# Performance work log

Hardware: AMD Instinct MI355X
Metric: run time of the kernel (lower is better)

Reference implementation:

```python
import jax, jax.numpy as jnp
import numpy as np

B, T, RNN_DIM, EMB_DIM, ATT_DIM = 64, 2048, 1024, 512, 128
N_FILT, KSIZE = 32, 31
PAD = (KSIZE - 1) // 2


def setup_inputs() -> dict:
    key = jax.random.key(0)
    ks = jax.random.split(key, 9)
    return {
        "attention_hidden_state": jax.random.normal(ks[0], (B, RNN_DIM), jnp.float32),
        "memory": jax.random.normal(ks[1], (B, T, EMB_DIM), jnp.float32),
        "processed_memory": jax.random.normal(ks[2], (B, T, ATT_DIM), jnp.float32),
        "attention_weights_cat": jax.random.uniform(ks[3], (B, 2, T), jnp.float32),
        "mask": jnp.zeros((B, T), dtype=bool),
        # learned params (torch Linear stores weight as (out, in))
        "Wq": jax.random.normal(ks[4], (ATT_DIM, RNN_DIM), jnp.float32) * 0.02,
        "conv_w": jax.random.normal(ks[5], (N_FILT, 2, KSIZE), jnp.float32) * 0.1,
        "Wd": jax.random.normal(ks[6], (ATT_DIM, N_FILT), jnp.float32) * 0.1,
        "v": jax.random.normal(ks[7], (1, ATT_DIM), jnp.float32) * 0.1,
    }


def reference(attention_hidden_state, memory, processed_memory,
              attention_weights_cat, mask, Wq, conv_w, Wd, v):
    # processed_query: (B, 1, ATT_DIM)
    pq = jnp.einsum('br,ar->ba', attention_hidden_state, Wq)[:, None, :]
    # location conv: (B, 2, T) -> (B, N_FILT, T), padding keeps length
    loc = jax.lax.conv_general_dilated(
        attention_weights_cat, conv_w,
        window_strides=(1,), padding=[(PAD, PAD)],
        dimension_numbers=('NCH', 'OIH', 'NCH'))
    # transpose to (B, T, N_FILT), dense to (B, T, ATT_DIM)
    loc = jnp.einsum('bft,af->bta', loc, Wd)
    # energies: tanh(pq + loc + pm) @ v^T -> (B, T)
    energies = jnp.einsum('bta,a->bt', jnp.tanh(pq + loc + processed_memory), v[0])
    energies = jnp.where(mask, -jnp.inf, energies)
    attention_weights = jax.nn.softmax(energies, axis=1)
    # context: (B, 1, T) x (B, T, EMB) -> (B, EMB)
    attention_context = jnp.einsum('bt,bte->be', attention_weights, memory)
    return attention_context, attention_weights
```

## Files before the change

### kernel.cpp

```cpp
#include <hip/hip_runtime.h>
#include <hip/hip_bf16.h>
#include <cstdint>

#define BB 64
#define TN 2048
#define RNN 1024
#define EMB 512
#define ATT 128
#define NF 32
#define KS 31
#define PADK 15
#define CKN 62
#define TT 256

__device__ __forceinline__ float fast_rcp(float x) {
#if __has_builtin(__builtin_amdgcn_rcpf)
    return __builtin_amdgcn_rcpf(x);
#else
    return 1.0f / x;
#endif
}

__device__ __forceinline__ float fast_tanh(float x) {
    float s = __expf(2.0f * x);
    return 1.0f - 2.0f * fast_rcp(s + 1.0f);
}

__global__ __launch_bounds__(256) void prep_kernel(
    const float* __restrict__ ahs, const float* __restrict__ Wq,
    const float* __restrict__ conv_w, const float* __restrict__ Wd,
    float* __restrict__ ws_pq, float* __restrict__ ws_U)
{
    int tid = threadIdx.x;
    if (blockIdx.x < BB) {
        int b = blockIdx.x;
        __shared__ float sh[RNN];
        for (int i = tid; i < RNN; i += 256) sh[i] = ahs[b * RNN + i];
        __syncthreads();
        int a = tid & 127, half = tid >> 7;
        const float4* wq4 = (const float4*)(Wq + a * RNN + half * (RNN / 2));
        const float4* sh4 = (const float4*)(sh + half * (RNN / 2));
        float acc = 0.0f;
#pragma unroll 8
        for (int i = 0; i < RNN / 8; ++i) {
            float4 w4 = wq4[i]; float4 h4 = sh4[i];
            acc = fmaf(w4.x, h4.x, acc);
            acc = fmaf(w4.y, h4.y, acc);
            acc = fmaf(w4.z, h4.z, acc);
            acc = fmaf(w4.w, h4.w, acc);
        }
        __shared__ float part[256];
        part[tid] = acc;
        __syncthreads();
        if (half == 0) ws_pq[b * ATT + a] = part[a] + part[a + 128];
    } else {
        __shared__ float sWd[ATT * NF];
        __shared__ float sCw[NF * CKN];
        for (int i = tid; i < ATT * NF; i += 256) sWd[i] = Wd[i];
        for (int i = tid; i < NF * CKN; i += 256) sCw[i] = conv_w[i];
        __syncthreads();
        for (int idx = tid; idx < ATT * CKN; idx += 256) {
            int a = idx / CKN, ck = idx % CKN;
            float acc = 0.0f;
#pragma unroll
            for (int f = 0; f < NF; ++f) acc = fmaf(sWd[a * NF + f], sCw[f * CKN + ck], acc);
            ws_U[idx] = acc;
        }
    }
}

__global__ __launch_bounds__(256) void energies_kernel(
    const float* __restrict__ awc, const float* __restrict__ pm,
    const float* __restrict__ vvec,
    const float* __restrict__ ws_pq, const float* __restrict__ ws_U,
    float* __restrict__ ws_e)
{
    __shared__ float sU[ATT * 63];
    __shared__ float sA[2][TT + 32];
    __shared__ float sPq[ATT];
    int tid = threadIdx.x;
    int b = blockIdx.x, t0 = blockIdx.y * TT;

    for (int idx = tid; idx < ATT * CKN; idx += 256) {
        int a = idx / CKN, ck = idx % CKN;
        sU[a * 63 + ck] = ws_U[idx];
    }
    for (int idx = tid; idx < 2 * (TT + 30); idx += 256) {
        int c = idx / (TT + 30), tt = idx % (TT + 30);
        int t = t0 + tt - PADK;
        sA[c][tt] = (t >= 0 && t < TN) ? awc[(b * 2 + c) * TN + t] : 0.0f;
    }
    if (tid < ATT) sPq[tid] = ws_pq[b * ATT + tid];
    __syncthreads();

    int lane = tid & 63, wv = tid >> 6;
    float v0 = vvec[lane], v1 = vvec[lane + 64];
    float q0 = sPq[lane], q1 = sPq[lane + 64];
    const float* U0 = &sU[lane * 63];
    const float* U1 = &sU[(lane + 64) * 63];
    const float* pmb = pm + (size_t)b * TN * ATT;

    for (int i = 0; i < TT / 4; ++i) {
        int tl = i * 4 + wv;
        int t = t0 + tl;
        float lo0 = 0.0f, lo1 = 0.0f;
#pragma unroll
        for (int c = 0; c < 2; ++c) {
#pragma unroll
            for (int k = 0; k < KS; ++k) {
                float x = sA[c][tl + k];
                lo0 = fmaf(U0[c * KS + k], x, lo0);
                lo1 = fmaf(U1[c * KS + k], x, lo1);
            }
        }
        float p0 = pmb[(size_t)t * ATT + lane];
        float p1 = pmb[(size_t)t * ATT + 64 + lane];
        float e = v0 * fast_tanh(q0 + lo0 + p0) + v1 * fast_tanh(q1 + lo1 + p1);
#pragma unroll
        for (int off = 32; off >= 1; off >>= 1) e += __shfl_xor(e, off, 64);
        if (lane == 0) ws_e[b * TN + t] = e;
    }
}

__global__ __launch_bounds__(256) void softmax_kernel(
    const float* __restrict__ ws_e, const uint8_t* __restrict__ mask,
    float* __restrict__ out_w)
{
    int b = blockIdx.x, tid = threadIdx.x;
    float vals[TN / 256];
    float m = -INFINITY;
#pragma unroll
    for (int i = 0; i < TN / 256; ++i) {
        int t = tid + i * 256;
        float e = ws_e[b * TN + t];
        if (mask[b * TN + t]) e = -INFINITY;
        vals[i] = e;
        m = fmaxf(m, e);
    }
    __shared__ float redm[4];
#pragma unroll
    for (int off = 32; off >= 1; off >>= 1) m = fmaxf(m, __shfl_xor(m, off, 64));
    if ((tid & 63) == 0) redm[tid >> 6] = m;
    __syncthreads();
    m = fmaxf(fmaxf(redm[0], redm[1]), fmaxf(redm[2], redm[3]));

    float s = 0.0f;
#pragma unroll
    for (int i = 0; i < TN / 256; ++i) s += __expf(vals[i] - m);
    __shared__ float reds[4];
#pragma unroll
    for (int off = 32; off >= 1; off >>= 1) s += __shfl_xor(s, off, 64);
    if ((tid & 63) == 0) reds[tid >> 6] = s;
    __syncthreads();
    s = reds[0] + reds[1] + reds[2] + reds[3];
    float inv = 1.0f / s;
#pragma unroll
    for (int i = 0; i < TN / 256; ++i) {
        int t = tid + i * 256;
        out_w[b * TN + t] = __expf(vals[i] - m) * inv;
    }
}

__global__ __launch_bounds__(256) void context_partial_kernel(
    const float* __restrict__ mem, const float* __restrict__ w,
    float* __restrict__ partial, int chunkT)
{
    int b = blockIdx.x, ch = blockIdx.y;
    int tid = threadIdx.x;
    int tc0 = ch * chunkT;
    extern __shared__ float sw[];
    for (int i = tid; i < chunkT; i += 256) sw[i] = w[b * TN + tc0 + i];
    __syncthreads();

    int e4 = tid & 127, sub = tid >> 7;
    const float4* m4 = (const float4*)(mem + ((size_t)(b * TN + tc0)) * EMB);
    float4 acc = make_float4(0.f, 0.f, 0.f, 0.f);
    for (int i = sub; i < chunkT; i += 2) {
        float wt = sw[i];
        float4 mv = m4[(size_t)i * 128 + e4];
        acc.x = fmaf(wt, mv.x, acc.x);
        acc.y = fmaf(wt, mv.y, acc.y);
        acc.z = fmaf(wt, mv.z, acc.z);
        acc.w = fmaf(wt, mv.w, acc.w);
    }
    __shared__ float4 sacc[128];
    if (sub == 1) sacc[e4] = acc;
    __syncthreads();
    if (sub == 0) {
        float4 o = sacc[e4];
        acc.x += o.x; acc.y += o.y; acc.z += o.z; acc.w += o.w;
        ((float4*)partial)[((size_t)ch * BB + b) * 128 + e4] = acc;
    }
}

__global__ __launch_bounds__(256) void context_reduce_kernel(
    const float* __restrict__ partial, float* __restrict__ out_ctx, int nchunk)
{
    int o = blockIdx.x * 256 + threadIdx.x;
    int b = o >> 9, e = o & 511;
    float acc = 0.0f;
    for (int c = 0; c < nchunk; ++c)
        acc += partial[((size_t)c * BB + b) * EMB + e];
    out_ctx[o] = acc;
}

extern "C" void kernel_launch(void* const* d_in, const int* in_sizes, int n_in,
                              void* d_out, int out_size, void* d_ws, size_t ws_size,
                              hipStream_t stream) {
    const float*   ahs  = (const float*)d_in[0];
    const float*   mem  = (const float*)d_in[1];
    const float*   pm   = (const float*)d_in[2];
    const float*   awc  = (const float*)d_in[3];
    const uint8_t* mask = (const uint8_t*)d_in[4];
    const float*   Wq   = (const float*)d_in[5];
    const float*   cw   = (const float*)d_in[6];
    const float*   Wd   = (const float*)d_in[7];
    const float*   v    = (const float*)d_in[8];

    float* out_ctx = (float*)d_out;
    float* out_w   = (float*)d_out + BB * EMB;

    float* ws      = (float*)d_ws;
    float* ws_pq   = ws;
    float* ws_U    = ws + 8192;
    float* ws_e    = ws + 16384;
    float* ws_part = ws + 147456;

    int nchunk = 16;
    while (nchunk > 1 &&
           (size_t)(147456 + (size_t)nchunk * BB * EMB) * 4 > ws_size)
        nchunk >>= 1;
    int chunkT = TN / nchunk;

    prep_kernel<<<BB + 1, 256, 0, stream>>>(ahs, Wq, cw, Wd, ws_pq, ws_U);
    energies_kernel<<<dim3(BB, TN / TT), 256, 0, stream>>>(awc, pm, v, ws_pq, ws_U, ws_e);
    softmax_kernel<<<BB, 256, 0, stream>>>(ws_e, mask, out_w);
    context_partial_kernel<<<dim3(BB, nchunk), 256, chunkT * 4, stream>>>(mem, out_w, ws_part, chunkT);
    context_reduce_kernel<<<(BB * EMB) / 256, 256, 0, stream>>>(ws_part, out_ctx, nchunk);
}
```

Baseline: 496.5 us.

## Register-cache conv weights in energies kernel and fuse softmax into context pass

The energies kernel now keeps each thread's 62 location-conv weights in registers from a transposed global layout, instead of staging the full U matrix in shared memory. Each wave handles one attention half and computes four timesteps per sliding window read from shared memory. Per-half energies are combined through shared memory. Softmax is merged into the context partial kernel: each block recomputes the row max and sum, then writes its own weight chunk, which removes one launch and the reload of the weights. The costs are redundant softmax reductions in every chunk block and higher register pressure, and the workspace-size fallback for the chunk count is dropped.

```diff
diff --git a/kernel.cpp b/kernel.cpp
--- a/kernel.cpp
+++ b/kernel.cpp
@@ -11,7 +11,9 @@
 #define KS 31
 #define PADK 15
 #define CKN 62
-#define TT 256
+#define ETT 256
+#define NCHUNK 16
+#define CHT 128
 
 __device__ __forceinline__ float fast_rcp(float x) {
 #if __has_builtin(__builtin_amdgcn_rcpf)
@@ -29,7 +31,7 @@
 __global__ __launch_bounds__(256) void prep_kernel(
     const float* __restrict__ ahs, const float* __restrict__ Wq,
     const float* __restrict__ conv_w, const float* __restrict__ Wd,
-    float* __restrict__ ws_pq, float* __restrict__ ws_U)
+    float* __restrict__ ws_pq, float* __restrict__ ws_UT)
 {
     int tid = threadIdx.x;
     if (blockIdx.x < BB) {
@@ -60,11 +62,11 @@
         for (int i = tid; i < NF * CKN; i += 256) sCw[i] = conv_w[i];
         __syncthreads();
         for (int idx = tid; idx < ATT * CKN; idx += 256) {
-            int a = idx / CKN, ck = idx % CKN;
+            int a = idx & 127, ck = idx >> 7;
             float acc = 0.0f;
 #pragma unroll
             for (int f = 0; f < NF; ++f) acc = fmaf(sWd[a * NF + f], sCw[f * CKN + ck], acc);
-            ws_U[idx] = acc;
+            ws_UT[idx] = acc;
         }
     }
 }
@@ -72,61 +74,69 @@
 __global__ __launch_bounds__(256) void energies_kernel(
     const float* __restrict__ awc, const float* __restrict__ pm,
     const float* __restrict__ vvec,
-    const float* __restrict__ ws_pq, const float* __restrict__ ws_U,
+    const float* __restrict__ ws_pq, const float* __restrict__ ws_UT,
     float* __restrict__ ws_e)
 {
-    __shared__ float sU[ATT * 63];
-    __shared__ float sA[2][TT + 32];
-    __shared__ float sPq[ATT];
+    __shared__ float sA[2][ETT + 32];
+    __shared__ float sE[2][ETT];
     int tid = threadIdx.x;
-    int b = blockIdx.x, t0 = blockIdx.y * TT;
-
-    for (int idx = tid; idx < ATT * CKN; idx += 256) {
-        int a = idx / CKN, ck = idx % CKN;
-        sU[a * 63 + ck] = ws_U[idx];
-    }
-    for (int idx = tid; idx < 2 * (TT + 30); idx += 256) {
-        int c = idx / (TT + 30), tt = idx % (TT + 30);
+    int b = blockIdx.x, t0 = blockIdx.y * ETT;
+
+    for (int idx = tid; idx < 2 * (ETT + 30); idx += 256) {
+        int c = idx / (ETT + 30), tt = idx % (ETT + 30);
         int t = t0 + tt - PADK;
         sA[c][tt] = (t >= 0 && t < TN) ? awc[(b * 2 + c) * TN + t] : 0.0f;
     }
-    if (tid < ATT) sPq[tid] = ws_pq[b * ATT + tid];
-    __syncthreads();
-
-    int lane = tid & 63, wv = tid >> 6;
-    float v0 = vvec[lane], v1 = vvec[lane + 64];
-    float q0 = sPq[lane], q1 = sPq[lane + 64];
-    const float* U0 = &sU[lane * 63];
-    const float* U1 = &sU[(lane + 64) * 63];
-    const float* pmb = pm + (size_t)b * TN * ATT;
-
-    for (int i = 0; i < TT / 4; ++i) {
-        int tl = i * 4 + wv;
-        int t = t0 + tl;
-        float lo0 = 0.0f, lo1 = 0.0f;
-#pragma unroll
-        for (int c = 0; c < 2; ++c) {
+
+    int lane = tid & 63, w = tid >> 6;
+    int h = w & 1, seg = w >> 1;
+    int a = h * 64 + lane;
+
+    float U[CKN];
+#pragma unroll
+    for (int k = 0; k < CKN; ++k) U[k] = ws_UT[k * ATT + a];
+    float q = ws_pq[b * ATT + a];
+    float vv = vvec[a];
+    const float* pmb = pm + (size_t)b * TN * ATT + a;
+    __syncthreads();
+
+    int tbeg = seg * (ETT / 2);
+    for (int tl = tbeg; tl < tbeg + ETT / 2; tl += 4) {
+        float xw0[34], xw1[34];
+#pragma unroll
+        for (int j = 0; j < 34; ++j) {
+            xw0[j] = sA[0][tl + j];
+            xw1[j] = sA[1][tl + j];
+        }
+        float p[4];
+#pragma unroll
+        for (int u = 0; u < 4; ++u)
+            p[u] = pmb[(size_t)(t0 + tl + u) * ATT];
+#pragma unroll
+        for (int u = 0; u < 4; ++u) {
+            float lo = 0.0f;
 #pragma unroll
             for (int k = 0; k < KS; ++k) {
-                float x = sA[c][tl + k];
-                lo0 = fmaf(U0[c * KS + k], x, lo0);
-                lo1 = fmaf(U1[c * KS + k], x, lo1);
+                lo = fmaf(U[k],      xw0[u + k], lo);
+                lo = fmaf(U[KS + k], xw1[u + k], lo);
             }
-        }
-        float p0 = pmb[(size_t)t * ATT + lane];
-        float p1 = pmb[(size_t)t * ATT + 64 + lane];
-        float e = v0 * fast_tanh(q0 + lo0 + p0) + v1 * fast_tanh(q1 + lo1 + p1);
-#pragma unroll
-        for (int off = 32; off >= 1; off >>= 1) e += __shfl_xor(e, off, 64);
-        if (lane == 0) ws_e[b * TN + t] = e;
-    }
-}
-
-__global__ __launch_bounds__(256) void softmax_kernel(
+            float e = vv * fast_tanh(q + lo + p[u]);
+#pragma unroll
+            for (int off = 32; off >= 1; off >>= 1) e += __shfl_xor(e, off, 64);
+            if (lane == 0) sE[h][tl + u] = e;
+        }
+    }
+    __syncthreads();
+    ws_e[b * TN + t0 + tid] = sE[0][tid] + sE[1][tid];
+}
+
+__global__ __launch_bounds__(256) void context_fused_kernel(
     const float* __restrict__ ws_e, const uint8_t* __restrict__ mask,
-    float* __restrict__ out_w)
-{
-    int b = blockIdx.x, tid = threadIdx.x;
+    const float* __restrict__ mem,
+    float* __restrict__ out_w, float* __restrict__ partial)
+{
+    int b = blockIdx.x, ch = blockIdx.y, tid = threadIdx.x;
+
     float vals[TN / 256];
     float m = -INFINITY;
 #pragma unroll
@@ -154,28 +164,23 @@
     __syncthreads();
     s = reds[0] + reds[1] + reds[2] + reds[3];
     float inv = 1.0f / s;
-#pragma unroll
-    for (int i = 0; i < TN / 256; ++i) {
-        int t = tid + i * 256;
-        out_w[b * TN + t] = __expf(vals[i] - m) * inv;
-    }
-}
-
-__global__ __launch_bounds__(256) void context_partial_kernel(
-    const float* __restrict__ mem, const float* __restrict__ w,
-    float* __restrict__ partial, int chunkT)
-{
-    int b = blockIdx.x, ch = blockIdx.y;
-    int tid = threadIdx.x;
-    int tc0 = ch * chunkT;
-    extern __shared__ float sw[];
-    for (int i = tid; i < chunkT; i += 256) sw[i] = w[b * TN + tc0 + i];
+
+    __shared__ float sw[CHT];
+    int tc0 = ch * CHT;
+    if (tid < CHT) {
+        int t = tc0 + tid;
+        float e = ws_e[b * TN + t];
+        if (mask[b * TN + t]) e = -INFINITY;
+        float wgt = __expf(e - m) * inv;
+        out_w[b * TN + t] = wgt;
+        sw[tid] = wgt;
+    }
     __syncthreads();
 
     int e4 = tid & 127, sub = tid >> 7;
     const float4* m4 = (const float4*)(mem + ((size_t)(b * TN + tc0)) * EMB);
     float4 acc = make_float4(0.f, 0.f, 0.f, 0.f);
-    for (int i = sub; i < chunkT; i += 2) {
+    for (int i = sub; i < CHT; i += 2) {
         float wt = sw[i];
         float4 mv = m4[(size_t)i * 128 + e4];
         acc.x = fmaf(wt, mv.x, acc.x);
@@ -194,12 +199,13 @@
 }
 
 __global__ __launch_bounds__(256) void context_reduce_kernel(
-    const float* __restrict__ partial, float* __restrict__ out_ctx, int nchunk)
+    const float* __restrict__ partial, float* __restrict__ out_ctx)
 {
     int o = blockIdx.x * 256 + threadIdx.x;
     int b = o >> 9, e = o & 511;
     float acc = 0.0f;
-    for (int c = 0; c < nchunk; ++c)
+#pragma unroll
+    for (int c = 0; c < NCHUNK; ++c)
         acc += partial[((size_t)c * BB + b) * EMB + e];
     out_ctx[o] = acc;
 }
@@ -222,19 +228,12 @@
 
     float* ws      = (float*)d_ws;
     float* ws_pq   = ws;
-    float* ws_U    = ws + 8192;
+    float* ws_UT   = ws + 8192;
     float* ws_e    = ws + 16384;
     float* ws_part = ws + 147456;
 
-    int nchunk = 16;
-    while (nchunk > 1 &&
-           (size_t)(147456 + (size_t)nchunk * BB * EMB) * 4 > ws_size)
-        nchunk >>= 1;
-    int chunkT = TN / nchunk;
-
-    prep_kernel<<<BB + 1, 256, 0, stream>>>(ahs, Wq, cw, Wd, ws_pq, ws_U);
-    energies_kernel<<<dim3(BB, TN / TT), 256, 0, stream>>>(awc, pm, v, ws_pq, ws_U, ws_e);
-    softmax_kernel<<<BB, 256, 0, stream>>>(ws_e, mask, out_w);
-    context_partial_kernel<<<dim3(BB, nchunk), 256, chunkT * 4, stream>>>(mem, out_w, ws_part, chunkT);
-    context_reduce_kernel<<<(BB * EMB) / 256, 256, 0, stream>>>(ws_part, out_ctx, nchunk);
-}
+    prep_kernel<<<BB + 1, 256, 0, stream>>>(ahs, Wq, cw, Wd, ws_pq, ws_UT);
+    energies_kernel<<<dim3(BB, TN / ETT), 256, 0, stream>>>(awc, pm, v, ws_pq, ws_UT, ws_e);
+    context_fused_kernel<<<dim3(BB, NCHUNK), 256, 0, stream>>>(ws_e, mask, mem, out_w, ws_part);
+    context_reduce_kernel<<<(BB * EMB) / 256, 256, 0, stream>>>(ws_part, out_ctx);
+}
```

Measured after the change: 477.0 us. 3.9% less time.
